# Performance work log

Hardware: AMD Instinct MI355X
Metric: run time of the kernel (lower is better)

The kernel has to match this reference:

```python
import jax, jax.numpy as jnp
import numpy as np

N = 10000      # atoms
E = 320000     # edges (~32 neighbors/atom)
H = 128        # hidden_channels
F = 128        # num_filters
R = 50         # num_rbf
L = 6          # num_layers
MAXZ = 100
CUT = 5.0      # cutoff_upper (cutoff_lower = 0)


def _cosine_cutoff(d):
    # CosineCutoff with lower=0: 0.5*(cos(pi*d/cut)+1) for d < cut, else 0
    return jnp.where(d < CUT, 0.5 * (jnp.cos(jnp.pi * d / CUT) + 1.0), 0.0)


def _xavier(k, shape):
    fan_in, fan_out = shape[-2], shape[-1]
    lim = np.sqrt(6.0 / (fan_in + fan_out)).astype(np.float32)
    return jax.random.uniform(k, shape, jnp.float32, -lim, lim)


def setup_inputs() -> dict:
    key = jax.random.key(0)
    ks = jax.random.split(key, 16)
    start = float(np.exp(-CUT))  # exp(-cutoff_upper + cutoff_lower)
    return {
        "z": jax.random.randint(ks[0], (N,), 0, MAXZ),
        "pos": jax.random.normal(ks[1], (N, 3), jnp.float32) * 3.0,
        "batch": jnp.zeros((N,), jnp.int32),
        "edge_index": jax.random.randint(ks[2], (2, E), 0, N),
        # nn.Embedding for atom types (main + NeighborEmbedding's own table)
        "emb_table": jax.random.normal(ks[3], (MAXZ, H), jnp.float32),
        "nbr_emb_table": jax.random.normal(ks[4], (MAXZ, H), jnp.float32),
        # NeighborEmbedding: distance_proj (R->H) and combine (2H->H)
        "nbr_proj_W": _xavier(ks[5], (R, H)),
        "nbr_proj_b": jnp.zeros((H,), jnp.float32),
        "nbr_comb_W": _xavier(ks[6], (2 * H, H)),
        "nbr_comb_b": jnp.zeros((H,), jnp.float32),
        # ExpNormalSmearing params (trainable)
        "rbf_means": jnp.linspace(start, 1.0, R, dtype=jnp.float32),
        "rbf_betas": jnp.full((R,), (2.0 / R * (1.0 - start)) ** -2, dtype=jnp.float32),
        # L interaction blocks, params stacked on leading layer dim
        "mlpW1": _xavier(ks[7], (L, R, F)),   # filter net lin1
        "mlpb1": jnp.zeros((L, F), jnp.float32),
        "mlpW2": _xavier(ks[8], (L, F, F)),   # filter net lin2
        "mlpb2": jnp.zeros((L, F), jnp.float32),
        "convW1": _xavier(ks[9], (L, H, F)),  # CFConv lin1 (no bias)
        "convW2": _xavier(ks[10], (L, F, H)), # CFConv lin2
        "convb2": jnp.zeros((L, H), jnp.float32),
        "linW": _xavier(ks[11], (L, H, H)),   # InteractionBlock final lin
        "linb": jnp.zeros((L, H), jnp.float32),
    }


def reference(z, pos, batch, edge_index, emb_table, nbr_emb_table,
              nbr_proj_W, nbr_proj_b, nbr_comb_W, nbr_comb_b,
              rbf_means, rbf_betas, mlpW1, mlpb1, mlpW2, mlpb2,
              convW1, convW2, convb2, linW, linb):
    src, dst = edge_index[0], edge_index[1]
    diff = pos[src] - pos[dst]                       # (E,3)
    d = jnp.sqrt(jnp.sum(diff * diff, axis=-1) + 1e-12)  # edge_weight (E,)
    C = _cosine_cutoff(d)                            # (E,)
    # ExpNormalSmearing: alpha = 5/(cut-0) = 1
    edge_attr = C[:, None] * jnp.exp(
        -rbf_betas * (jnp.exp(-d)[:, None] - rbf_means) ** 2)  # (E,R)

    x = emb_table[z]                                 # (N,H)

    # NeighborEmbedding: self-loops removed, filter modulated by cutoff
    mask = (src != dst).astype(x.dtype)
    Wn = (edge_attr @ nbr_proj_W + nbr_proj_b) * (C * mask)[:, None]  # (E,H)
    msg = jax.ops.segment_sum(nbr_emb_table[z][src] * Wn, dst, num_segments=N)
    x = jnp.concatenate([x, msg], axis=-1) @ nbr_comb_W + nbr_comb_b

    # Interaction blocks: CFConv (gather - filter-MLP - scatter) + residual
    for l in range(L):
        Wf = jax.nn.silu(edge_attr @ mlpW1[l] + mlpb1[l]) @ mlpW2[l] + mlpb2[l]
        Wf = Wf * C[:, None]                         # (E,F)
        y = x @ convW1[l]                            # (N,F), no bias
        m = jax.ops.segment_sum(y[src] * Wf, dst, num_segments=N)  # aggr='add'
        y = jax.nn.silu(m @ convW2[l] + convb2[l])
        y = y @ linW[l] + linb[l]
        x = x + y
    return x
```

## Files before the change

kernel.cpp:

```cpp
#include <hip/hip_runtime.h>
#include <hip/hip_bf16.h>


#define NATOMS 10000
#define NEDGES 320000
#define HC 128
#define RBF 50
#define NLAY 6
#define MAXZ_ 100
#define NK 8192
#define EG 1250
#define TBGRID (7 * (NK / 64))
#define EGRID (NEDGES / 64)
#define YGRID ((NATOMS + 63) / 64)
#define UGRID (NATOMS / 16)

typedef __hip_bfloat16 bf16;
typedef __attribute__((ext_vector_type(8))) short bf8v;
typedef __attribute__((ext_vector_type(4))) float f4v;

__device__ __forceinline__ float b2f(bf16 v) { return __bfloat162float(v); }
__device__ __forceinline__ bf16  f2b(float v) { return __float2bfloat16(v); }
__device__ __forceinline__ short f2s(float v) { bf16 h = f2b(v); return *(short*)&h; }
__device__ __forceinline__ float s2f(unsigned short s) {
    return __int_as_float(((int)s) << 16);
}
__device__ __forceinline__ float silu(float v) {
    return v * __builtin_amdgcn_rcpf(1.0f + __expf(-v));
}
__device__ __forceinline__ int isf_of(const int* flagp) {
    return (__int_as_float(flagp[0]) > 1.0e4f) ? 1 : 0;
}

template<int ISF>
__device__ __forceinline__ float LD(const void* p, size_t i) {
    if (ISF) return ((const float*)p)[i];
    return b2f(((const bf16*)p)[i]);
}

__device__ __forceinline__ bf8v f32x8_to_b(const float* p) {
    f4v v0 = *(const f4v*)p;
    f4v v1 = *(const f4v*)(p + 4);
    bf8v r;
    r[0] = f2s(v0[0]); r[1] = f2s(v0[1]); r[2] = f2s(v0[2]); r[3] = f2s(v0[3]);
    r[4] = f2s(v1[0]); r[5] = f2s(v1[1]); r[6] = f2s(v1[2]); r[7] = f2s(v1[3]);
    return r;
}
template<int ISF>
__device__ __forceinline__ bf8v LD8(const void* p, size_t i) {
    if (ISF) return f32x8_to_b((const float*)p + i);
    return *(const bf8v*)((const bf16*)p + i);
}

__device__ __forceinline__ int clampN(int v) {
    return v < 0 ? 0 : (v >= NATOMS ? NATOMS - 1 : v);
}

template<int ISF>
__device__ __forceinline__ float edge_d(const int* __restrict__ ei,
                                        const void* __restrict__ pos, int e,
                                        int* sOut, int* tOut) {
    int s = clampN(ei[e]);
    int t = clampN(ei[NEDGES + e]);
    *sOut = s; *tOut = t;
    float dx = LD<ISF>(pos, (size_t)s * 3 + 0) - LD<ISF>(pos, (size_t)t * 3 + 0);
    float dy = LD<ISF>(pos, (size_t)s * 3 + 1) - LD<ISF>(pos, (size_t)t * 3 + 1);
    float dz = LD<ISF>(pos, (size_t)s * 3 + 2) - LD<ISF>(pos, (size_t)t * 3 + 2);
    float d = sqrtf(dx * dx + dy * dy + dz * dz + 1e-12f);
    if (d != d) d = 1e30f;
    return d;
}

__global__ void probe_k(const void* pos, int* flag) {
    int i = blockIdx.x * 256 + threadIdx.x;
    float v = 0.0f;
    if (i < NATOMS * 3) {
        v = fabsf(b2f(((const bf16*)pos)[i]));
        if (v != v) v = 1e30f;
    }
    #pragma unroll
    for (int off = 32; off > 0; off >>= 1)
        v = fmaxf(v, __shfl_xor(v, off, 64));
    if ((threadIdx.x & 63) == 0) atomicMax(flag, __float_as_int(v));
}

template<int ISF>
__device__ __forceinline__ void histd_body(int b, int tid, const int* __restrict__ ei,
                                           const void* __restrict__ pos,
                                           int* __restrict__ counts,
                                           float* __restrict__ d_raw) {
    int e = b * 256 + tid;
    if (e >= NEDGES) return;
    int s, t;
    float d = edge_d<ISF>(ei, pos, e, &s, &t);
    d_raw[e] = d;
    if (d < 5.0f) atomicAdd(&counts[t], 1);
}

template<int ISF>
__device__ void packB_at(int t, const void* src, int K, int ksteps, size_t perLsrc,
                         size_t perLdst, int L, bf16* dst) {
    if (t >= L * 8 * ksteps * 64) return;
    int lane = t & 63;
    int t2 = t >> 6;
    int ks = t2 % ksteps;
    int t3 = t2 / ksteps;
    int nt = t3 & 7;
    int l  = t3 >> 3;
    int quad = lane >> 4, lc = lane & 15;
    int col = nt * 16 + lc;
    for (int j = 0; j < 8; j++) {
        int k = ks * 32 + quad * 8 + j;
        float v = (k < K) ? LD<ISF>(src, (size_t)l * perLsrc + (size_t)k * 128 + col) : 0.0f;
        dst[(size_t)l * perLdst + ((size_t)((nt * ksteps + ks) * 64 + lane)) * 8 + j] = f2b(v);
    }
}
template<int ISF>
__device__ void packB24_at(int t, const void* w2, const void* cw1, const void* cw2,
                           const void* lw, bf16* w2p, bf16* cw1p, bf16* cw2p, bf16* lwp) {
    if (t >= 24 * 8 * 4 * 64) return;
    int lane = t & 63;
    int t2 = t >> 6;
    int ks = t2 & 3;
    int t3 = t2 >> 2;
    int nt = t3 & 7;
    int m  = t3 >> 3;
    int which = m / NLAY, li = m % NLAY;
    const void* src = which == 0 ? w2 : which == 1 ? cw1 : which == 2 ? cw2 : lw;
    bf16* dst = which == 0 ? w2p : which == 1 ? cw1p : which == 2 ? cw2p : lwp;
    int quad = lane >> 4, lc = lane & 15;
    int col = nt * 16 + lc;
    #pragma unroll
    for (int j = 0; j < 8; j++) {
        int k = ks * 32 + quad * 8 + j;
        float v = LD<ISF>(src, (size_t)li * 16384 + (size_t)k * 128 + col);
        dst[(size_t)li * 16384 + ((size_t)((nt * 4 + ks) * 64 + lane)) * 8 + j] = f2b(v);
    }
}
template<int ISF>
__device__ void cvts_at(int i, const void* means, const void* betas, const void* bp,
                        const void* bc, const void* b1, const void* b2,
                        const void* cb2, const void* lb,
                        float* meanscv, float* betascv, float* bpcv, float* bccv,
                        float* b1cv, float* b2cv, float* cb2cv, float* lbcv) {
    if      (i < 50)   meanscv[i]        = LD<ISF>(means, i);
    else if (i < 100)  betascv[i - 50]   = LD<ISF>(betas, i - 50);
    else if (i < 228)  bpcv[i - 100]     = LD<ISF>(bp, i - 100);
    else if (i < 356)  bccv[i - 228]     = LD<ISF>(bc, i - 228);
    else if (i < 1124) b1cv[i - 356]     = LD<ISF>(b1, i - 356);
    else if (i < 1892) b2cv[i - 1124]    = LD<ISF>(b2, i - 1124);
    else if (i < 2660) cb2cv[i - 1892]   = LD<ISF>(cb2, i - 1892);
    else if (i < 3428) lbcv[i - 2660]    = LD<ISF>(lb, i - 2660);
}
template<int ISF>
__device__ void packall_body(int b, int tid, const void* Wp, const void* Wc, const void* W1,
                             const void* W2, const void* cW1, const void* cW2,
                             const void* lW, const void* means, const void* betas,
                             const void* bp, const void* bc, const void* b1,
                             const void* b2, const void* cb2, const void* lb,
                             const void* nbremb,
                             bf16* wpp, bf16* wcp, bf16* w1p, bf16* w2p, bf16* cw1p,
                             bf16* cw2p, bf16* lwp, float* meanscv, float* betascv,
                             float* bpcv, float* bccv, float* b1cv, float* b2cv,
                             float* cb2cv, float* lbcv, bf16* nbrembbf) {
    if (b < 4)        packB_at<ISF>(b * 256 + tid, Wp, RBF, 2, 6400, 8192, 1, wpp);
    else if (b < 20)  packB_at<ISF>((b - 4) * 256 + tid, Wc, 256, 8, 32768, 32768, 1, wcp);
    else if (b < 44)  packB_at<ISF>((b - 20) * 256 + tid, W1, RBF, 2, 6400, 8192, NLAY, w1p);
    else if (b < 236) packB24_at<ISF>((b - 44) * 256 + tid, W2, cW1, cW2, lW,
                                      w2p, cw1p, cw2p, lwp);
    else if (b < 250) cvts_at<ISF>((b - 236) * 256 + tid, means, betas, bp, bc, b1, b2,
                                   cb2, lb, meanscv, betascv, bpcv, bccv,
                                   b1cv, b2cv, cb2cv, lbcv);
    else {
        int i = (b - 250) * 256 + tid;
        if (i < MAXZ_ * HC) nbrembbf[i] = f2b(LD<ISF>(nbremb, i));
    }
}

__global__ __launch_bounds__(256)
void setup1_k(const int* ei, const void* pos, const int* flagp,
              int* counts, float* d_raw,
              const void* Wp, const void* Wc, const void* W1,
              const void* W2, const void* cW1, const void* cW2,
              const void* lW, const void* means, const void* betas,
              const void* bp, const void* bc, const void* b1,
              const void* b2, const void* cb2, const void* lb,
              const void* nbremb,
              bf16* wpp, bf16* wcp, bf16* w1p, bf16* w2p, bf16* cw1p,
              bf16* cw2p, bf16* lwp, float* meanscv, float* betascv,
              float* bpcv, float* bccv, float* b1cv, float* b2cv,
              float* cb2cv, float* lbcv, bf16* nbrembbf) {
    int b = blockIdx.x, tid = threadIdx.x;
    int isf = isf_of(flagp);
    if (b < EG) {
        if (isf) histd_body<1>(b, tid, ei, pos, counts, d_raw);
        else     histd_body<0>(b, tid, ei, pos, counts, d_raw);
    } else {
        b -= EG;
        if (isf) packall_body<1>(b, tid, Wp, Wc, W1, W2, cW1, cW2, lW, means, betas,
                                 bp, bc, b1, b2, cb2, lb, nbremb, wpp, wcp,
                                 w1p, w2p, cw1p, cw2p, lwp, meanscv, betascv,
                                 bpcv, bccv, b1cv, b2cv, cb2cv, lbcv, nbrembbf);
        else     packall_body<0>(b, tid, Wp, Wc, W1, W2, cW1, cW2, lW, means, betas,
                                 bp, bc, b1, b2, cb2, lb, nbremb, wpp, wcp,
                                 w1p, w2p, cw1p, cw2p, lwp, meanscv, betascv,
                                 bpcv, bccv, b1cv, b2cv, cb2cv, lbcv, nbrembbf);
    }
}

__global__ void scan_k(const int* __restrict__ counts, int* __restrict__ rowptr,
                       int* __restrict__ cursor) {
    __shared__ int wsum[16];
    int tid = threadIdx.x, lane = tid & 63, w = tid >> 6;
    int base = tid * 10;
    int v[10];
    int s = 0;
    #pragma unroll
    for (int j = 0; j < 10; j++) {
        int i = base + j;
        int c = (i < NATOMS) ? counts[i] : 0;
        v[j] = c; s += c;
    }
    int si = s;
    #pragma unroll
    for (int off = 1; off < 64; off <<= 1) {
        int t = __shfl_up(si, off, 64);
        if (lane >= off) si += t;
    }
    if (lane == 63) wsum[w] = si;
    __syncthreads();
    if (w == 0 && lane < 16) {
        int t = wsum[lane];
        int s2 = t;
        #pragma unroll
        for (int off = 1; off < 16; off <<= 1) {
            int u = __shfl_up(s2, off, 64);
            if (lane >= off) s2 += u;
        }
        wsum[lane] = s2 - t;
    }
    __syncthreads();
    int run = wsum[w] + si - s;
    #pragma unroll
    for (int j = 0; j < 10; j++) {
        int i = base + j;
        if (i < NATOMS) {
            cursor[i] = run;
            run += v[j];
            rowptr[i + 1] = run;
        }
    }
    if (tid == 0) rowptr[0] = 0;
}

#define MFMA(a, b, c) __builtin_amdgcn_mfma_f32_16x16x32_bf16((a), (b), (c), 0, 0, 0)

__device__ __forceinline__ void permgeom_body(int b, int tid, const int* __restrict__ ei,
                                              const float* __restrict__ d_raw,
                                              int* __restrict__ cursor,
                                              float* __restrict__ ed_s,
                                              int* __restrict__ src_s,
                                              int* __restrict__ dst_s) {
    int e = b * 256 + tid;
    if (e >= NEDGES) return;
    float d = d_raw[e];
    if (d >= 5.0f) return;
    int s = clampN(ei[e]);
    int t = clampN(ei[NEDGES + e]);
    int p = atomicAdd(&cursor[t], 1);
    ed_s[p] = __expf(-d);
    src_s[p] = s;
    dst_s[p] = t;
}

__device__ __forceinline__ void tabbuild_body(int bb, int tid,
                const bf16* __restrict__ wpp, const float* __restrict__ bpcv,
                const bf16* __restrict__ w1p, const float* __restrict__ b1cv,
                const bf16* __restrict__ w2p, const float* __restrict__ b2cv,
                const float* __restrict__ meanscv, const float* __restrict__ betascv,
                bf16* __restrict__ Tb) {
    __shared__ bf16 hid[64][136];
    __shared__ float csh[64], edsh[64];
    int f = bb >> 7, kb = bb & 127;
    int base = kb * 64;
    int wave = tid >> 6, lane = tid & 63, quad = lane >> 4, lc = lane & 15;
    if (tid < 64) {
        float ed = (float)(base + tid) * (1.0f / (NK - 1));
        float d = -logf(fmaxf(ed, 1e-30f));
        float C = (d < 5.0f) ? 0.5f * (__cosf(d * 0.6283185307f) + 1.0f) : 0.0f;
        csh[tid] = C; edsh[tid] = ed;
    }
    __syncthreads();
    float edi = edsh[wave * 16 + lc], Ci = csh[wave * 16 + lc];
    bf8v af[2];
    #pragma unroll
    for (int ks = 0; ks < 2; ks++) {
        #pragma unroll
        for (int j = 0; j < 8; j++) {
            int r = ks * 32 + quad * 8 + j;
            float v = 0.0f;
            if (r < RBF) { float u = edi - meanscv[r]; v = Ci * __expf(-betascv[r] * u * u); }
            af[ks][j] = f2s(v);
        }
    }
    f4v zero = {0.f, 0.f, 0.f, 0.f};
    f4v acc[8];
    #pragma unroll
    for (int nt = 0; nt < 8; nt++) acc[nt] = zero;
    const bf16* w1b = (f == 0) ? wpp : w1p + (size_t)(f - 1) * 8192;
    #pragma unroll
    for (int nt = 0; nt < 8; nt++)
        #pragma unroll
        for (int ks = 0; ks < 2; ks++) {
            bf8v b = *(const bf8v*)(w1b + ((nt * 2 + ks) * 64 + lane) * 8);
            acc[nt] = MFMA(af[ks], b, acc[nt]);
        }
    if (f == 0) {
        #pragma unroll
        for (int nt = 0; nt < 8; nt++) {
            int n = nt * 16 + lc;
            float bb2 = bpcv[n];
            #pragma unroll
            for (int r = 0; r < 4; r++) {
                int row = wave * 16 + quad * 4 + r;
                Tb[(size_t)(base + row) * HC + n] = f2b((acc[nt][r] + bb2) * csh[row]);
            }
        }
        return;
    }
    int l = f - 1;
    #pragma unroll
    for (int nt = 0; nt < 8; nt++) {
        int n = nt * 16 + lc;
        float bb2 = b1cv[l * HC + n];
        #pragma unroll
        for (int r = 0; r < 4; r++)
            hid[wave * 16 + quad * 4 + r][n] = f2b(silu(acc[nt][r] + bb2));
    }
    __syncthreads();
    bf8v a2[4];
    #pragma unroll
    for (int ks = 0; ks < 4; ks++)
        a2[ks] = *(const bf8v*)&hid[wave * 16 + lc][ks * 32 + quad * 8];
    f4v acc2[8];
    #pragma unroll
    for (int nt = 0; nt < 8; nt++) acc2[nt] = zero;
    const bf16* w2b = w2p + (size_t)l * 16384;
    #pragma unroll
    for (int nt = 0; nt < 8; nt++)
        #pragma unroll
        for (int ks = 0; ks < 4; ks++) {
            bf8v b = *(const bf8v*)(w2b + ((nt * 4 + ks) * 64 + lane) * 8);
            acc2[nt] = MFMA(a2[ks], b, acc2[nt]);
        }
    #pragma unroll
    for (int nt = 0; nt < 8; nt++) {
        int n = nt * 16 + lc;
        float bb2 = b2cv[l * HC + n];
        #pragma unroll
        for (int r = 0; r < 4; r++) {
            int row = wave * 16 + quad * 4 + r;
            Tb[((size_t)f * NK + base + row) * HC + n] = f2b((acc2[nt][r] + bb2) * csh[row]);
        }
    }
}

__global__ __launch_bounds__(256)
void setup2_k(const int* ei, const float* d_raw, int* cursor,
              float* ed_s, int* src_s, int* dst_s,
              const bf16* wpp, const float* bpcv,
              const bf16* w1p, const float* b1cv,
              const bf16* w2p, const float* b2cv,
              const float* meanscv, const float* betascv, bf16* Tb) {
    int b = blockIdx.x, tid = threadIdx.x;
    if (b < EG) permgeom_body(b, tid, ei, d_raw, cursor, ed_s, src_s, dst_s);
    else        tabbuild_body(b - EG, tid, wpp, bpcv, w1p, b1cv, w2p, b2cv,
                              meanscv, betascv, Tb);
}

__device__ __forceinline__ void seg_prep(const int* __restrict__ dst_s, int i0, int tid,
                                         int* ddst, int* slot_s, int* distinct_s,
                                         int* nseg_s) {
    if (tid < 64) {
        int d = dst_s[i0 + tid];
        ddst[tid] = d;
        int dprev = __shfl_up(d, 1, 64);
        int flag = (tid == 0 || d != dprev) ? 1 : 0;
        int s = flag;
        #pragma unroll
        for (int off = 1; off < 64; off <<= 1) {
            int t = __shfl_up(s, off, 64);
            if (tid >= off) s += t;
        }
        slot_s[tid] = s - 1;
        if (flag) distinct_s[s - 1] = d;
        if (tid == 63) *nseg_s = s;
    }
}

__device__ __forceinline__ void seg_mfma(const bf16 (*mvT)[72], const int* ddst,
                                         const int* slot_s, const int* distinct_s,
                                         int nseg, float* __restrict__ out, int tid) {
    int wave = tid >> 6, lane = tid & 63, quad = lane >> 4, lc = lane & 15;
    if (nseg <= 16) {
        bf8v sa[2];
        #pragma unroll
        for (int ks = 0; ks < 2; ks++)
            #pragma unroll
            for (int j = 0; j < 8; j++) {
                int k = ks * 32 + quad * 8 + j;
                sa[ks][j] = (slot_s[k] == lc) ? (short)0x3F80 : (short)0;
            }
        f4v z4 = {0.f, 0.f, 0.f, 0.f};
        f4v sacc[2] = {z4, z4};
        #pragma unroll
        for (int nt = 0; nt < 2; nt++)
            #pragma unroll
            for (int ks = 0; ks < 2; ks++) {
                bf8v b = *(const bf8v*)&mvT[wave * 32 + nt * 16 + lc][ks * 32 + quad * 8];
                sacc[nt] = MFMA(sa[ks], b, sacc[nt]);
            }
        #pragma unroll
        for (int nt = 0; nt < 2; nt++)
            #pragma unroll
            for (int r = 0; r < 4; r++) {
                int sl = quad * 4 + r;
                if (sl < nseg) {
                    int atom = distinct_s[sl];
                    int n = wave * 32 + nt * 16 + lc;
                    float v = sacc[nt][r];
                    if (sl == 0 || sl == nseg - 1)
                        atomicAdd(&out[(size_t)atom * HC + n], v);
                    else
                        out[(size_t)atom * HC + n] = v;
                }
            }
    } else {
        int col = tid & 127;
        int base = (tid >> 7) * 32;
        int cur = ddst[base];
        float s = 0.0f;
        bool first = true;
        for (int e = base; e < base + 32; e++) {
            int dn = ddst[e];
            if (dn != cur) {
                if (first) atomicAdd(&out[(size_t)cur * HC + col], s);
                else out[(size_t)cur * HC + col] = s;
                first = false; cur = dn; s = 0.0f;
            }
            s += b2f(mvT[col][e]);
        }
        atomicAdd(&out[(size_t)cur * HC + col], s);
    }
}

__global__ __launch_bounds__(256)
void nbr_tab_k(const int* __restrict__ rowptr,
               const float* __restrict__ ed_s, const int* __restrict__ src_s,
               const int* __restrict__ dst_s, const int* __restrict__ z,
               const bf16* __restrict__ nbrembbf, const bf16* __restrict__ Tb,
               float* __restrict__ msg) {
    __shared__ bf16 mvT[128][72];
    __shared__ int ddst[64], slot_s[64], distinct_s[64];
    __shared__ int nseg_s;
    int i0 = blockIdx.x * 64;
    if (i0 >= rowptr[NATOMS]) return;
    int tid = threadIdx.x;
    seg_prep(dst_s, i0, tid, ddst, slot_s, distinct_s, &nseg_s);
    int row = tid & 63, c0 = (tid >> 6) * 32;
    int e = i0 + row;
    int s = src_s[e];
    float msk = (s != dst_s[e]) ? 1.0f : 0.0f;
    float pos = fminf(fmaxf(ed_s[e] * (float)(NK - 1) + 0.5f, 0.0f), (float)(NK - 1));
    int k = (int)pos;
    const bf8v* tp = (const bf8v*)(Tb + (size_t)k * HC + c0);
    bf8v tv[4];
    #pragma unroll
    for (int g = 0; g < 4; g++) tv[g] = tp[g];
    int zz = z[s]; zz = zz < 0 ? 0 : (zz >= MAXZ_ ? MAXZ_ - 1 : zz);
    const bf8v* ep = (const bf8v*)(nbrembbf + (size_t)zz * HC + c0);
    bf8v ev[4];
    #pragma unroll
    for (int g = 0; g < 4; g++) ev[g] = ep[g];
    #pragma unroll
    for (int g = 0; g < 4; g++)
        #pragma unroll
        for (int m = 0; m < 8; m++) {
            float v = s2f((unsigned short)tv[g][m]) * msk *
                      s2f((unsigned short)ev[g][m]);
            mvT[c0 + g * 8 + m][row] = f2b(v);
        }
    __syncthreads();
    seg_mfma(mvT, ddst, slot_s, distinct_s, nseg_s, msg, tid);
}

template<int ISF>
__device__ void combine_body(const int* __restrict__ z, const void* __restrict__ emb,
                             const float* __restrict__ msg, const bf16* __restrict__ wcp,
                             const float* __restrict__ bccv, const bf16* __restrict__ cw1b,
                             float* __restrict__ x, bf16* __restrict__ xb,
                             bf16* __restrict__ ybf) {
    __shared__ bf16 srow[64][136];
    int tid = threadIdx.x;
    int wave = tid >> 6, lane = tid & 63, quad = lane >> 4, lc = lane & 15;
    int m0 = blockIdx.x * 64;
    int arow = m0 + wave * 16 + lc;
    int rowc = arow < NATOMS ? arow : NATOMS - 1;
    int zz = z[rowc]; zz = zz < 0 ? 0 : (zz >= MAXZ_ ? MAXZ_ - 1 : zz);
    bf8v af[8];
    #pragma unroll
    for (int ks = 0; ks < 4; ks++)
        af[ks] = LD8<ISF>(emb, (size_t)zz * HC + ks * 32 + quad * 8);
    #pragma unroll
    for (int ks = 4; ks < 8; ks++)
        af[ks] = f32x8_to_b(msg + (size_t)rowc * HC + (ks - 4) * 32 + quad * 8);
    f4v zero = {0.f, 0.f, 0.f, 0.f};
    f4v acc[8];
    #pragma unroll
    for (int nt = 0; nt < 8; nt++) acc[nt] = zero;
    #pragma unroll
    for (int nt = 0; nt < 8; nt++)
        #pragma unroll
        for (int ks = 0; ks < 8; ks++) {
            bf8v b = *(const bf8v*)(wcp + ((nt * 8 + ks) * 64 + lane) * 8);
            acc[nt] = MFMA(af[ks], b, acc[nt]);
        }
    #pragma unroll
    for (int nt = 0; nt < 8; nt++) {
        int n = nt * 16 + lc;
        float bb = bccv[n];
        #pragma unroll
        for (int r = 0; r < 4; r++) {
            int row = m0 + wave * 16 + quad * 4 + r;
            float v = acc[nt][r] + bb;
            bf16 vb = f2b(v);
            srow[wave * 16 + quad * 4 + r][n] = vb;
            if (row < NATOMS) {
                x[(size_t)row * HC + n] = v;
                xb[(size_t)row * HC + n] = vb;
            }
        }
    }
    __syncthreads();
    bf8v a3[4];
    #pragma unroll
    for (int ks = 0; ks < 4; ks++)
        a3[ks] = *(const bf8v*)&srow[wave * 16 + lc][ks * 32 + quad * 8];
    f4v acc3[8];
    #pragma unroll
    for (int nt = 0; nt < 8; nt++) acc3[nt] = zero;
    #pragma unroll
    for (int nt = 0; nt < 8; nt++)
        #pragma unroll
        for (int ks = 0; ks < 4; ks++) {
            bf8v b = *(const bf8v*)(cw1b + ((nt * 4 + ks) * 64 + lane) * 8);
            acc3[nt] = MFMA(a3[ks], b, acc3[nt]);
        }
    #pragma unroll
    for (int nt = 0; nt < 8; nt++) {
        int n = nt * 16 + lc;
        #pragma unroll
        for (int r = 0; r < 4; r++) {
            int row = m0 + wave * 16 + quad * 4 + r;
            if (row < NATOMS) ybf[(size_t)row * HC + n] = f2b(acc3[nt][r]);
        }
    }
}
__global__ __launch_bounds__(256)
void combine_k(const int* z, const void* emb, const float* msg, const bf16* wcp,
               const float* bccv, const bf16* cw1b, const int* flagp,
               float* x, bf16* xb, bf16* ybf) {
    if (isf_of(flagp)) combine_body<1>(z, emb, msg, wcp, bccv, cw1b, x, xb, ybf);
    else               combine_body<0>(z, emb, msg, wcp, bccv, cw1b, x, xb, ybf);
}

__global__ __launch_bounds__(256)
void filt_tab_k(int l, const int* __restrict__ rowptr,
                const float* __restrict__ ed_s, const int* __restrict__ src_s,
                const int* __restrict__ dst_s, const bf16* __restrict__ ybf,
                const bf16* __restrict__ Tb, float* __restrict__ msum) {
    __shared__ bf16 mvT[128][72];
    __shared__ int ddst[64], slot_s[64], distinct_s[64];
    __shared__ int nseg_s;
    int i0 = blockIdx.x * 64;
    if (i0 >= rowptr[NATOMS]) return;
    int tid = threadIdx.x;
    seg_prep(dst_s, i0, tid, ddst, slot_s, distinct_s, &nseg_s);
    int row = tid & 63, c0 = (tid >> 6) * 32;
    int e = i0 + row;
    float pos = fminf(fmaxf(ed_s[e] * (float)(NK - 1) + 0.5f, 0.0f), (float)(NK - 1));
    int k = (int)pos;
    const bf8v* tp = (const bf8v*)(Tb + ((size_t)(l + 1) * NK + k) * HC + c0);
    bf8v tv[4];
    #pragma unroll
    for (int g = 0; g < 4; g++) tv[g] = tp[g];
    const bf8v* yp = (const bf8v*)(ybf + (size_t)src_s[e] * HC + c0);
    bf8v yv[4];
    #pragma unroll
    for (int g = 0; g < 4; g++) yv[g] = yp[g];
    #pragma unroll
    for (int g = 0; g < 4; g++)
        #pragma unroll
        for (int m = 0; m < 8; m++) {
            float v = s2f((unsigned short)tv[g][m]) * s2f((unsigned short)yv[g][m]);
            mvT[c0 + g * 8 + m][row] = f2b(v);
        }
    __syncthreads();
    seg_mfma(mvT, ddst, slot_s, distinct_s, nseg_s, msum, tid);
}

__global__ __launch_bounds__(256)
void upd_mfma_k(float* msum, int l,
                const bf16* __restrict__ cw2p, const float* __restrict__ cb2cv,
                const bf16* __restrict__ lwp, const float* __restrict__ lbcv,
                const bf16* __restrict__ cw1p, int do_y, int last,
                float* __restrict__ x, bf16* __restrict__ xb,
                bf16* __restrict__ ybf, void* out, const int* flagp) {
    __shared__ bf16 srow[16][136];
    int tid = threadIdx.x;
    int w = tid >> 6, lane = tid & 63, quad = lane >> 4, lc = lane & 15;
    int m0 = blockIdx.x * 16;
    bf8v af[4];
    #pragma unroll
    for (int ks = 0; ks < 4; ks++)
        af[ks] = f32x8_to_b(msum + (size_t)(m0 + lc) * HC + ks * 32 + quad * 8);
    f4v zero = {0.f, 0.f, 0.f, 0.f};
    f4v acc[2] = {zero, zero};
    const bf16* c2b = cw2p + (size_t)l * 16384;
    #pragma unroll
    for (int nt = 0; nt < 2; nt++)
        #pragma unroll
        for (int ks = 0; ks < 4; ks++) {
            bf8v b = *(const bf8v*)(c2b + (((w * 2 + nt) * 4 + ks) * 64 + lane) * 8);
            acc[nt] = MFMA(af[ks], b, acc[nt]);
        }
    #pragma unroll
    for (int nt = 0; nt < 2; nt++) {
        int n = w * 32 + nt * 16 + lc;
        float bb = cb2cv[l * HC + n];
        #pragma unroll
        for (int r = 0; r < 4; r++)
            srow[quad * 4 + r][n] = f2b(silu(acc[nt][r] + bb));
    }
    __syncthreads();
    {
        int zr = tid >> 4, zc = (tid & 15) * 8;
        *(f4v*)(msum + (size_t)(m0 + zr) * HC + zc) = zero;
        *(f4v*)(msum + (size_t)(m0 + zr) * HC + zc + 4) = zero;
    }
    bf8v a2[4];
    #pragma unroll
    for (int ks = 0; ks < 4; ks++)
        a2[ks] = *(const bf8v*)&srow[lc][ks * 32 + quad * 8];
    __syncthreads();
    f4v acc2[2] = {zero, zero};
    const bf16* lwb = lwp + (size_t)l * 16384;
    #pragma unroll
    for (int nt = 0; nt < 2; nt++)
        #pragma unroll
        for (int ks = 0; ks < 4; ks++) {
            bf8v b = *(const bf8v*)(lwb + (((w * 2 + nt) * 4 + ks) * 64 + lane) * 8);
            acc2[nt] = MFMA(a2[ks], b, acc2[nt]);
        }
    int isf = isf_of(flagp);
    #pragma unroll
    for (int nt = 0; nt < 2; nt++) {
        int n = w * 32 + nt * 16 + lc;
        float bb = lbcv[l * HC + n];
        #pragma unroll
        for (int r = 0; r < 4; r++) {
            int row = m0 + quad * 4 + r;
            size_t o = (size_t)row * HC + n;
            float nv = x[o] + acc2[nt][r] + bb;
            if (!last) {
                x[o] = nv;
                xb[o] = f2b(nv);
            } else {
                if (isf) ((float*)out)[o] = nv;
                else     ((bf16*)out)[o] = f2b(nv);
            }
            srow[quad * 4 + r][n] = f2b(nv);
        }
    }
    if (do_y) {
        __syncthreads();
        bf8v a3[4];
        #pragma unroll
        for (int ks = 0; ks < 4; ks++)
            a3[ks] = *(const bf8v*)&srow[lc][ks * 32 + quad * 8];
        f4v acc3[2] = {zero, zero};
        const bf16* c1b = cw1p + (size_t)(l + 1) * 16384;
        #pragma unroll
        for (int nt = 0; nt < 2; nt++)
            #pragma unroll
            for (int ks = 0; ks < 4; ks++) {
                bf8v b = *(const bf8v*)(c1b + (((w * 2 + nt) * 4 + ks) * 64 + lane) * 8);
                acc3[nt] = MFMA(a3[ks], b, acc3[nt]);
            }
        #pragma unroll
        for (int nt = 0; nt < 2; nt++) {
            int n = w * 32 + nt * 16 + lc;
            #pragma unroll
            for (int r = 0; r < 4; r++) {
                int row = m0 + quad * 4 + r;
                ybf[(size_t)row * HC + n] = f2b(acc3[nt][r]);
            }
        }
    }
}

extern "C" void kernel_launch(void* const* d_in, const int* in_sizes, int n_in,
                              void* d_out, int out_size, void* d_ws, size_t ws_size,
                              hipStream_t stream) {
    const int*  z      = (const int*) d_in[0];
    const void* pos    = d_in[1];
    const int*  ei     = (const int*) d_in[3];
    const void* emb    = d_in[4];
    const void* nbremb = d_in[5];
    const void* Wp     = d_in[6];
    const void* bp     = d_in[7];
    const void* Wc     = d_in[8];
    const void* bc     = d_in[9];
    const void* means  = d_in[10];
    const void* betas  = d_in[11];
    const void* W1     = d_in[12];
    const void* b1     = d_in[13];
    const void* W2     = d_in[14];
    const void* b2     = d_in[15];
    const void* cW1    = d_in[16];
    const void* cW2    = d_in[17];
    const void* cb2    = d_in[18];
    const void* lW     = d_in[19];
    const void* lb     = d_in[20];

    char* p = (char*)d_ws;
    auto alloc = [&](size_t bytes) { char* r = p; p += (bytes + 255) / 256 * 256; return r; };
    int*   flag    = (int*)  alloc(256);
    int*   counts  = (int*)  alloc((size_t)NATOMS * 4);
    float* msum    = (float*)alloc((size_t)NATOMS * HC * 4);
    float* msg     = (float*)alloc((size_t)NATOMS * HC * 4);
    float* ed_s    = (float*)alloc((size_t)NEDGES * 4);
    int*   src_s   = (int*)  alloc((size_t)NEDGES * 4);
    int*   dst_s   = (int*)  alloc((size_t)NEDGES * 4);
    char*  zend    = p;
    int*   rowptr  = (int*)  alloc((size_t)(NATOMS + 1) * 4);
    int*   cursor  = (int*)  alloc((size_t)NATOMS * 4);
    float* d_raw   = (float*)alloc((size_t)NEDGES * 4);
    float* x       = (float*)alloc((size_t)NATOMS * HC * 4);
    bf16*  xb      = (bf16*) alloc((size_t)NATOMS * HC * 2);
    bf16*  ybf     = (bf16*) alloc((size_t)NATOMS * HC * 2);
    bf16*  Tb      = (bf16*) alloc((size_t)(NLAY + 1) * NK * HC * 2);
    bf16*  wpp     = (bf16*) alloc((size_t)8192 * 2);
    bf16*  wcp     = (bf16*) alloc((size_t)32768 * 2);
    bf16*  w1p     = (bf16*) alloc((size_t)NLAY * 8192 * 2);
    bf16*  w2p     = (bf16*) alloc((size_t)NLAY * 16384 * 2);
    bf16*  cw1p    = (bf16*) alloc((size_t)NLAY * 16384 * 2);
    bf16*  cw2p    = (bf16*) alloc((size_t)NLAY * 16384 * 2);
    bf16*  lwp     = (bf16*) alloc((size_t)NLAY * 16384 * 2);
    bf16*  nbrembbf= (bf16*) alloc((size_t)MAXZ_ * HC * 2);
    float* bpcv    = (float*)alloc((size_t)HC * 4);
    float* bccv    = (float*)alloc((size_t)HC * 4);
    float* b1cv    = (float*)alloc((size_t)NLAY * HC * 4);
    float* b2cv    = (float*)alloc((size_t)NLAY * HC * 4);
    float* cb2cv   = (float*)alloc((size_t)NLAY * HC * 4);
    float* lbcv    = (float*)alloc((size_t)NLAY * HC * 4);
    float* meanscv = (float*)alloc((size_t)RBF * 4);
    float* betascv = (float*)alloc((size_t)RBF * 4);

    hipMemsetAsync(flag, 0, (size_t)(zend - (char*)flag), stream);
    probe_k<<<(NATOMS * 3 + 255) / 256, 256, 0, stream>>>(pos, flag);

    setup1_k<<<EG + 300, 256, 0, stream>>>(ei, pos, flag, counts, d_raw,
                                           Wp, Wc, W1, W2, cW1, cW2, lW, means, betas,
                                           bp, bc, b1, b2, cb2, lb, nbremb,
                                           wpp, wcp, w1p, w2p, cw1p, cw2p, lwp,
                                           meanscv, betascv, bpcv, bccv, b1cv, b2cv,
                                           cb2cv, lbcv, nbrembbf);
    scan_k<<<1, 1024, 0, stream>>>(counts, rowptr, cursor);
    setup2_k<<<EG + TBGRID, 256, 0, stream>>>(ei, d_raw, cursor, ed_s, src_s, dst_s,
                                              wpp, bpcv, w1p, b1cv, w2p, b2cv,
                                              meanscv, betascv, Tb);

    nbr_tab_k<<<EGRID, 256, 0, stream>>>(rowptr, ed_s, src_s, dst_s, z, nbrembbf, Tb, msg);
    combine_k<<<YGRID, 256, 0, stream>>>(z, emb, msg, wcp, bccv, cw1p, flag, x, xb, ybf);

    for (int l = 0; l < NLAY; l++) {
        filt_tab_k<<<EGRID, 256, 0, stream>>>(l, rowptr, ed_s, src_s, dst_s, ybf, Tb, msum);
        int lastl = (l == NLAY - 1) ? 1 : 0;
        upd_mfma_k<<<UGRID, 256, 0, stream>>>(msum, l, cw2p, cb2cv, lwp, lbcv,
                                              cw1p, lastl ? 0 : 1, lastl,
                                              x, xb, ybf, d_out, flag);
    }
}
```

Before: 333.5 us.

## Cache segment metadata and table indices; use grid-stride persistent edge kernels

```diff
diff --git a/kernel.cpp b/kernel.cpp
--- a/kernel.cpp
+++ b/kernel.cpp
@@ -11,7 +11,8 @@
 #define NK 8192
 #define EG 1250
 #define TBGRID (7 * (NK / 64))
-#define EGRID (NEDGES / 64)
+#define NWIN (NEDGES / 64)
+#define EGGRID 2048
 #define YGRID ((NATOMS + 63) / 64)
 #define UGRID (NATOMS / 16)
 
@@ -258,7 +259,7 @@
 __device__ __forceinline__ void permgeom_body(int b, int tid, const int* __restrict__ ei,
                                               const float* __restrict__ d_raw,
                                               int* __restrict__ cursor,
-                                              float* __restrict__ ed_s,
+                                              int* __restrict__ kidx_s,
                                               int* __restrict__ src_s,
                                               int* __restrict__ dst_s) {
     int e = b * 256 + tid;
@@ -268,7 +269,9 @@
     int s = clampN(ei[e]);
     int t = clampN(ei[NEDGES + e]);
     int p = atomicAdd(&cursor[t], 1);
-    ed_s[p] = __expf(-d);
+    float ed = __expf(-d);
+    float pos = fminf(fmaxf(ed * (float)(NK - 1) + 0.5f, 0.0f), (float)(NK - 1));
+    kidx_s[p] = (int)pos;
     src_s[p] = s;
     dst_s[p] = t;
 }
@@ -367,13 +370,13 @@
 
 __global__ __launch_bounds__(256)
 void setup2_k(const int* ei, const float* d_raw, int* cursor,
-              float* ed_s, int* src_s, int* dst_s,
+              int* kidx_s, int* src_s, int* dst_s,
               const bf16* wpp, const float* bpcv,
               const bf16* w1p, const float* b1cv,
               const bf16* w2p, const float* b2cv,
               const float* meanscv, const float* betascv, bf16* Tb) {
     int b = blockIdx.x, tid = threadIdx.x;
-    if (b < EG) permgeom_body(b, tid, ei, d_raw, cursor, ed_s, src_s, dst_s);
+    if (b < EG) permgeom_body(b, tid, ei, d_raw, cursor, kidx_s, src_s, dst_s);
     else        tabbuild_body(b - EG, tid, wpp, bpcv, w1p, b1cv, w2p, b2cv,
                               meanscv, betascv, Tb);
 }
@@ -456,42 +459,52 @@
 
 __global__ __launch_bounds__(256)
 void nbr_tab_k(const int* __restrict__ rowptr,
-               const float* __restrict__ ed_s, const int* __restrict__ src_s,
+               const int* __restrict__ kidx_s, const int* __restrict__ src_s,
                const int* __restrict__ dst_s, const int* __restrict__ z,
                const bf16* __restrict__ nbrembbf, const bf16* __restrict__ Tb,
-               float* __restrict__ msg) {
+               float* __restrict__ msg,
+               int* __restrict__ slotb, int* __restrict__ distb,
+               int* __restrict__ ddstb, int* __restrict__ nsegb) {
     __shared__ bf16 mvT[128][72];
     __shared__ int ddst[64], slot_s[64], distinct_s[64];
     __shared__ int nseg_s;
-    int i0 = blockIdx.x * 64;
-    if (i0 >= rowptr[NATOMS]) return;
     int tid = threadIdx.x;
-    seg_prep(dst_s, i0, tid, ddst, slot_s, distinct_s, &nseg_s);
-    int row = tid & 63, c0 = (tid >> 6) * 32;
-    int e = i0 + row;
-    int s = src_s[e];
-    float msk = (s != dst_s[e]) ? 1.0f : 0.0f;
-    float pos = fminf(fmaxf(ed_s[e] * (float)(NK - 1) + 0.5f, 0.0f), (float)(NK - 1));
-    int k = (int)pos;
-    const bf8v* tp = (const bf8v*)(Tb + (size_t)k * HC + c0);
-    bf8v tv[4];
-    #pragma unroll
-    for (int g = 0; g < 4; g++) tv[g] = tp[g];
-    int zz = z[s]; zz = zz < 0 ? 0 : (zz >= MAXZ_ ? MAXZ_ - 1 : zz);
-    const bf8v* ep = (const bf8v*)(nbrembbf + (size_t)zz * HC + c0);
-    bf8v ev[4];
-    #pragma unroll
-    for (int g = 0; g < 4; g++) ev[g] = ep[g];
-    #pragma unroll
-    for (int g = 0; g < 4; g++)
-        #pragma unroll
-        for (int m = 0; m < 8; m++) {
-            float v = s2f((unsigned short)tv[g][m]) * msk *
-                      s2f((unsigned short)ev[g][m]);
-            mvT[c0 + g * 8 + m][row] = f2b(v);
-        }
-    __syncthreads();
-    seg_mfma(mvT, ddst, slot_s, distinct_s, nseg_s, msg, tid);
+    int Eact = rowptr[NATOMS];
+    for (int w = blockIdx.x; w * 64 < Eact; w += (int)gridDim.x) {
+        int i0 = w * 64;
+        seg_prep(dst_s, i0, tid, ddst, slot_s, distinct_s, &nseg_s);
+        if (tid < 64) {
+            ddstb[i0 + tid] = ddst[tid];
+            slotb[i0 + tid] = slot_s[tid];
+            distb[i0 + tid] = distinct_s[tid];
+            if (tid == 63) nsegb[w] = nseg_s;
+        }
+        int row = tid & 63, c0 = (tid >> 6) * 32;
+        int e = i0 + row;
+        int s = src_s[e];
+        float msk = (s != dst_s[e]) ? 1.0f : 0.0f;
+        int k = kidx_s[e];
+        const bf8v* tp = (const bf8v*)(Tb + (size_t)k * HC + c0);
+        bf8v tv[4];
+        #pragma unroll
+        for (int g = 0; g < 4; g++) tv[g] = tp[g];
+        int zz = z[s]; zz = zz < 0 ? 0 : (zz >= MAXZ_ ? MAXZ_ - 1 : zz);
+        const bf8v* ep = (const bf8v*)(nbrembbf + (size_t)zz * HC + c0);
+        bf8v ev[4];
+        #pragma unroll
+        for (int g = 0; g < 4; g++) ev[g] = ep[g];
+        #pragma unroll
+        for (int g = 0; g < 4; g++)
+            #pragma unroll
+            for (int m = 0; m < 8; m++) {
+                float v = s2f((unsigned short)tv[g][m]) * msk *
+                          s2f((unsigned short)ev[g][m]);
+                mvT[c0 + g * 8 + m][row] = f2b(v);
+            }
+        __syncthreads();
+        seg_mfma(mvT, ddst, slot_s, distinct_s, nseg_s, msg, tid);
+        __syncthreads();
+    }
 }
 
 template<int ISF>
@@ -576,37 +589,46 @@
 
 __global__ __launch_bounds__(256)
 void filt_tab_k(int l, const int* __restrict__ rowptr,
-                const float* __restrict__ ed_s, const int* __restrict__ src_s,
-                const int* __restrict__ dst_s, const bf16* __restrict__ ybf,
-                const bf16* __restrict__ Tb, float* __restrict__ msum) {
+                const int* __restrict__ kidx_s, const int* __restrict__ src_s,
+                const bf16* __restrict__ ybf, const bf16* __restrict__ Tb,
+                float* __restrict__ msum,
+                const int* __restrict__ slotb, const int* __restrict__ distb,
+                const int* __restrict__ ddstb, const int* __restrict__ nsegb) {
     __shared__ bf16 mvT[128][72];
     __shared__ int ddst[64], slot_s[64], distinct_s[64];
     __shared__ int nseg_s;
-    int i0 = blockIdx.x * 64;
-    if (i0 >= rowptr[NATOMS]) return;
     int tid = threadIdx.x;
-    seg_prep(dst_s, i0, tid, ddst, slot_s, distinct_s, &nseg_s);
-    int row = tid & 63, c0 = (tid >> 6) * 32;
-    int e = i0 + row;
-    float pos = fminf(fmaxf(ed_s[e] * (float)(NK - 1) + 0.5f, 0.0f), (float)(NK - 1));
-    int k = (int)pos;
-    const bf8v* tp = (const bf8v*)(Tb + ((size_t)(l + 1) * NK + k) * HC + c0);
-    bf8v tv[4];
-    #pragma unroll
-    for (int g = 0; g < 4; g++) tv[g] = tp[g];
-    const bf8v* yp = (const bf8v*)(ybf + (size_t)src_s[e] * HC + c0);
-    bf8v yv[4];
-    #pragma unroll
-    for (int g = 0; g < 4; g++) yv[g] = yp[g];
-    #pragma unroll
-    for (int g = 0; g < 4; g++)
-        #pragma unroll
-        for (int m = 0; m < 8; m++) {
-            float v = s2f((unsigned short)tv[g][m]) * s2f((unsigned short)yv[g][m]);
-            mvT[c0 + g * 8 + m][row] = f2b(v);
-        }
-    __syncthreads();
-    seg_mfma(mvT, ddst, slot_s, distinct_s, nseg_s, msum, tid);
+    int Eact = rowptr[NATOMS];
+    for (int w = blockIdx.x; w * 64 < Eact; w += (int)gridDim.x) {
+        int i0 = w * 64;
+        if (tid < 64) {
+            ddst[tid] = ddstb[i0 + tid];
+            slot_s[tid] = slotb[i0 + tid];
+            distinct_s[tid] = distb[i0 + tid];
+            if (tid == 0) nseg_s = nsegb[w];
+        }
+        int row = tid & 63, c0 = (tid >> 6) * 32;
+        int e = i0 + row;
+        int k = kidx_s[e];
+        const bf8v* tp = (const bf8v*)(Tb + ((size_t)(l + 1) * NK + k) * HC + c0);
+        bf8v tv[4];
+        #pragma unroll
+        for (int g = 0; g < 4; g++) tv[g] = tp[g];
+        const bf8v* yp = (const bf8v*)(ybf + (size_t)src_s[e] * HC + c0);
+        bf8v yv[4];
+        #pragma unroll
+        for (int g = 0; g < 4; g++) yv[g] = yp[g];
+        #pragma unroll
+        for (int g = 0; g < 4; g++)
+            #pragma unroll
+            for (int m = 0; m < 8; m++) {
+                float v = s2f((unsigned short)tv[g][m]) * s2f((unsigned short)yv[g][m]);
+                mvT[c0 + g * 8 + m][row] = f2b(v);
+            }
+        __syncthreads();
+        seg_mfma(mvT, ddst, slot_s, distinct_s, nseg_s, msum, tid);
+        __syncthreads();
+    }
 }
 
 __global__ __launch_bounds__(256)
@@ -739,13 +761,17 @@
     int*   counts  = (int*)  alloc((size_t)NATOMS * 4);
     float* msum    = (float*)alloc((size_t)NATOMS * HC * 4);
     float* msg     = (float*)alloc((size_t)NATOMS * HC * 4);
-    float* ed_s    = (float*)alloc((size_t)NEDGES * 4);
+    int*   kidx_s  = (int*)  alloc((size_t)NEDGES * 4);
     int*   src_s   = (int*)  alloc((size_t)NEDGES * 4);
     int*   dst_s   = (int*)  alloc((size_t)NEDGES * 4);
     char*  zend    = p;
     int*   rowptr  = (int*)  alloc((size_t)(NATOMS + 1) * 4);
     int*   cursor  = (int*)  alloc((size_t)NATOMS * 4);
     float* d_raw   = (float*)alloc((size_t)NEDGES * 4);
+    int*   slotb   = (int*)  alloc((size_t)NEDGES * 4);
+    int*   distb   = (int*)  alloc((size_t)NEDGES * 4);
+    int*   ddstb   = (int*)  alloc((size_t)NEDGES * 4);
+    int*   nsegb   = (int*)  alloc((size_t)NWIN * 4);
     float* x       = (float*)alloc((size_t)NATOMS * HC * 4);
     bf16*  xb      = (bf16*) alloc((size_t)NATOMS * HC * 2);
     bf16*  ybf     = (bf16*) alloc((size_t)NATOMS * HC * 2);
@@ -777,15 +803,17 @@
                                            meanscv, betascv, bpcv, bccv, b1cv, b2cv,
                                            cb2cv, lbcv, nbrembbf);
     scan_k<<<1, 1024, 0, stream>>>(counts, rowptr, cursor);
-    setup2_k<<<EG + TBGRID, 256, 0, stream>>>(ei, d_raw, cursor, ed_s, src_s, dst_s,
+    setup2_k<<<EG + TBGRID, 256, 0, stream>>>(ei, d_raw, cursor, kidx_s, src_s, dst_s,
                                               wpp, bpcv, w1p, b1cv, w2p, b2cv,
                                               meanscv, betascv, Tb);
 
-    nbr_tab_k<<<EGRID, 256, 0, stream>>>(rowptr, ed_s, src_s, dst_s, z, nbrembbf, Tb, msg);
+    nbr_tab_k<<<EGGRID, 256, 0, stream>>>(rowptr, kidx_s, src_s, dst_s, z, nbrembbf,
+                                          Tb, msg, slotb, distb, ddstb, nsegb);
     combine_k<<<YGRID, 256, 0, stream>>>(z, emb, msg, wcp, bccv, cw1p, flag, x, xb, ybf);
 
     for (int l = 0; l < NLAY; l++) {
-        filt_tab_k<<<EGRID, 256, 0, stream>>>(l, rowptr, ed_s, src_s, dst_s, ybf, Tb, msum);
+        filt_tab_k<<<EGGRID, 256, 0, stream>>>(l, rowptr, kidx_s, src_s, ybf, Tb, msum,
+                                               slotb, distb, ddstb, nsegb);
         int lastl = (l == NLAY - 1) ? 1 : 0;
         upd_mfma_k<<<UGRID, 256, 0, stream>>>(msum, l, cw2p, cb2cv, lwp, lbcv,
                                               cw1p, lastl ? 0 : 1, lastl,
```

Result: slower. 343.8 us (+3.1%).
